# Kernel optimization log

Measured on AMD Instinct MI355X. Metric: run time of the kernel, lower is better.

The kernel has to match this reference:

```python
import jax, jax.numpy as jnp
import numpy as np

SEQ = 4096
EMBED = 1024


def setup_inputs() -> dict:
    key = jax.random.key(0)
    k1, k2 = jax.random.split(key)
    x = jax.random.normal(k1, (SEQ, EMBED), dtype=jnp.float32)
    # torch Linear(embed, 3*embed): store transposed weight so y = x @ W + b
    W = jax.random.normal(k2, (EMBED, 3 * EMBED), dtype=jnp.float32) * (1.0 / np.sqrt(EMBED))
    b = jnp.zeros((3 * EMBED,), dtype=jnp.float32)
    return {"x": x, "W": W, "b": b}


def reference(x, W, b):
    # QKV projection: [S, 3E] -> chunk along features
    qkv = x @ W + b
    q, k, v = jnp.split(qkv, 3, axis=1)  # each [S, E]
    d = q.shape[-1]
    scale = jnp.sqrt(jnp.asarray(d, dtype=x.dtype))
    logits = (q @ k.T) / scale  # [S, S]
    S = q.shape[0]
    causal = jnp.triu(jnp.ones((S, S), dtype=bool), k=1)
    logits = jnp.where(causal, -jnp.inf, logits)
    w = jax.nn.softmax(logits, axis=1)
    return w @ v  # [S, E]
```

## Files before the change

kernel.cpp:

```cpp
#include <hip/hip_runtime.h>

typedef short s16x8 __attribute__((ext_vector_type(8)));
typedef unsigned short u16;
typedef u16 u16x8 __attribute__((ext_vector_type(8)));
typedef float f32x4 __attribute__((ext_vector_type(4)));

#define SEQ 4096
#define EMBED 1024
#define NQKV 3072

static __device__ __forceinline__ u16 f2bf(float f) {
  unsigned int u = __float_as_uint(f);
  u += 0x7fffu + ((u >> 16) & 1u);
  return (u16)(u >> 16);
}
static __device__ __forceinline__ float bf2f(u16 b) {
  return __uint_as_float(((unsigned int)b) << 16);
}

static __device__ __forceinline__ f32x4 mfma16(s16x8 a, s16x8 b, f32x4 c) {
  return __builtin_amdgcn_mfma_f32_16x16x32_bf16(a, b, c, 0, 0, 0);
}

static __device__ __forceinline__ void gl2lds(const u16* g, u16* l) {
  __builtin_amdgcn_global_load_lds(
      (const __attribute__((address_space(1))) unsigned int*)g,
      (__attribute__((address_space(3))) unsigned int*)l, 16, 0, 0);
}

#define WAITVM(n) asm volatile("s_waitcnt vmcnt(" #n ")" ::: "memory")
#define LGKM0 asm volatile("s_waitcnt lgkmcnt(0)" ::: "memory")
#define BAR() asm volatile("s_waitcnt lgkmcnt(0)\n\ts_barrier" ::: "memory")

__global__ __launch_bounds__(256) void conv_x(const float* __restrict__ x,
                                              u16* __restrict__ xbf) {
  const size_t base = ((size_t)blockIdx.x * 256 + threadIdx.x) * 16;
  u16 tmp[16];
#pragma unroll
  for (int p = 0; p < 4; ++p) {
    float4 v = *reinterpret_cast<const float4*>(&x[base + p * 4]);
    tmp[p * 4 + 0] = f2bf(v.x); tmp[p * 4 + 1] = f2bf(v.y);
    tmp[p * 4 + 2] = f2bf(v.z); tmp[p * 4 + 3] = f2bf(v.w);
  }
  *reinterpret_cast<u16x8*>(&xbf[base]) = *reinterpret_cast<u16x8*>(&tmp[0]);
  *reinterpret_cast<u16x8*>(&xbf[base + 8]) = *reinterpret_cast<u16x8*>(&tmp[8]);
}

__global__ __launch_bounds__(256) void conv_wT(const float* __restrict__ W,
                                               u16* __restrict__ wT) {
  __shared__ u16 t[64][72];
  const int n0 = blockIdx.x * 64;
  const int k0 = blockIdx.y * 64;
  const int tid = threadIdx.x;
  const int rr = tid >> 3, c8 = (tid & 7) * 8;
#pragma unroll
  for (int p = 0; p < 2; ++p) {
    int r = p * 32 + rr;
    float4 a = *reinterpret_cast<const float4*>(&W[(size_t)(k0 + r) * NQKV + n0 + c8]);
    float4 b = *reinterpret_cast<const float4*>(&W[(size_t)(k0 + r) * NQKV + n0 + c8 + 4]);
    t[r][c8 + 0] = f2bf(a.x); t[r][c8 + 1] = f2bf(a.y);
    t[r][c8 + 2] = f2bf(a.z); t[r][c8 + 3] = f2bf(a.w);
    t[r][c8 + 4] = f2bf(b.x); t[r][c8 + 5] = f2bf(b.y);
    t[r][c8 + 6] = f2bf(b.z); t[r][c8 + 7] = f2bf(b.w);
  }
  __syncthreads();
#pragma unroll
  for (int p = 0; p < 2; ++p) {
    int c = p * 32 + rr;
    u16x8 v;
#pragma unroll
    for (int j = 0; j < 8; ++j) v[j] = t[c8 + j][c];
    *reinterpret_cast<u16x8*>(&wT[(size_t)(n0 + c) * EMBED + k0 + c8]) = v;
  }
}

#define GSTAGE32(dst, srcbase, stride)                                        \
  {                                                                           \
    _Pragma("unroll") for (int p_ = 0; p_ < 2; ++p_) {                        \
      gl2lds((srcbase) + (size_t)(p_ * 64 + w * 16 + (l >> 2)) * (stride) +   \
                 (l & 3) * 8,                                                 \
             (dst) + p_ * 2048 + w * 512);                                    \
    }                                                                         \
  }

#define MFMA_STEP(Acur, Bcur)                                                 \
  {                                                                           \
    s16x8 af[4], bfr[4];                                                      \
    _Pragma("unroll") for (int mb = 0; mb < 4; ++mb)                          \
        af[mb] = *reinterpret_cast<const s16x8*>(&(Acur)[(wr + mb * 16 + lr) * 32 + lg * 8]); \
    _Pragma("unroll") for (int nb = 0; nb < 4; ++nb)                          \
        bfr[nb] = *reinterpret_cast<const s16x8*>(&(Bcur)[(wc + nb * 16 + lr) * 32 + lg * 8]); \
    _Pragma("unroll") for (int mb = 0; mb < 4; ++mb)                          \
        _Pragma("unroll") for (int nb = 0; nb < 4; ++nb)                      \
            acc[mb][nb] = mfma16(af[mb], bfr[nb], acc[mb][nb]);               \
  }

__global__ __launch_bounds__(256) void qkv_gemm(const u16* __restrict__ xbf,
                                                const u16* __restrict__ wT,
                                                const float* __restrict__ bias,
                                                u16* __restrict__ qkv) {
  __shared__ u16 As[2][4096];
  __shared__ u16 Bs[2][4096];
  const int b = blockIdx.x;
  const int bs = (b & 7) * 96 + (b >> 3);
  const int bm = bs / 24, bn = bs % 24;
  const int m0 = bm * 128, n0 = bn * 128;
  const int tid = threadIdx.x;
  const int w = tid >> 6, l = tid & 63;
  const int wr = (w >> 1) * 64, wc = (w & 1) * 64;
  const int lg = l >> 4, lr = l & 15;

  f32x4 acc[4][4];
#pragma unroll
  for (int i = 0; i < 4; ++i)
#pragma unroll
    for (int j = 0; j < 4; ++j) acc[i][j] = (f32x4){0.f, 0.f, 0.f, 0.f};

  const u16* xa = xbf + (size_t)m0 * EMBED;
  const u16* wb = wT + (size_t)n0 * EMBED;

  GSTAGE32(As[0], xa, EMBED);
  GSTAGE32(Bs[0], wb, EMBED);

  for (int t = 0; t < 32; ++t) {
    const int cur = t & 1, nx = cur ^ 1;
    if (t < 31) {
      LGKM0;
      GSTAGE32(As[nx], xa + (t + 1) * 32, EMBED);
      GSTAGE32(Bs[nx], wb + (t + 1) * 32, EMBED);
      WAITVM(4);
    } else {
      WAITVM(0);
    }
    BAR();
    MFMA_STEP(As[cur], Bs[cur]);
    BAR();
  }

#pragma unroll
  for (int mb = 0; mb < 4; ++mb)
#pragma unroll
    for (int nb = 0; nb < 4; ++nb) {
      const int col = n0 + wc + nb * 16 + lr;
      const float bv = bias[col];
#pragma unroll
      for (int e = 0; e < 4; ++e) {
        const int row = m0 + wr + mb * 16 + lg * 4 + e;
        qkv[(size_t)row * NQKV + col] = f2bf(acc[mb][nb][e] + bv);
      }
    }
}

__global__ __launch_bounds__(256) void v_transpose(const u16* __restrict__ qkv,
                                                   u16* __restrict__ vT) {
  __shared__ u16 t[64][72];
  const int s0 = blockIdx.x * 64;
  const int c0 = blockIdx.y * 64;
  const int tid = threadIdx.x;
  const int rr = tid >> 3, c8 = (tid & 7) * 8;
#pragma unroll
  for (int p = 0; p < 2; ++p) {
    int r = p * 32 + rr;
    *reinterpret_cast<u16x8*>(&t[r][c8]) =
        *reinterpret_cast<const u16x8*>(&qkv[(size_t)(s0 + r) * NQKV + 2 * EMBED + c0 + c8]);
  }
  __syncthreads();
#pragma unroll
  for (int p = 0; p < 2; ++p) {
    int c = p * 32 + rr;
    u16x8 v;
#pragma unroll
    for (int j = 0; j < 8; ++j) v[j] = t[c8 + j][c];
    *reinterpret_cast<u16x8*>(&vT[(size_t)(c0 + c) * SEQ + s0 + c8]) = v;
  }
}

__global__ __launch_bounds__(256) void s_gemm(const u16* __restrict__ qkv,
                                              u16* __restrict__ Sp) {
  __shared__ u16 As[2][4096];
  __shared__ u16 Bs[2][4096];
  const int b = blockIdx.x;
  const int bs = (b & 7) * 66 + (b >> 3);
  int mt = 0, cum = 0;
  while (cum + mt + 1 <= bs) { cum += mt + 1; ++mt; }
  const int nt = bs - cum;
  const int m0 = mt * 128, n0 = nt * 128;
  const int tid = threadIdx.x;
  const int w = tid >> 6, l = tid & 63;
  const int wr = (w >> 1) * 64, wc = (w & 1) * 64;
  const int lg = l >> 4, lr = l & 15;

  f32x4 acc[4][4];
#pragma unroll
  for (int i = 0; i < 4; ++i)
#pragma unroll
    for (int j = 0; j < 4; ++j) acc[i][j] = (f32x4){0.f, 0.f, 0.f, 0.f};

  const u16* qa = qkv + (size_t)m0 * NQKV;
  const u16* kb = qkv + (size_t)n0 * NQKV + EMBED;

  GSTAGE32(As[0], qa, NQKV);
  GSTAGE32(Bs[0], kb, NQKV);

  for (int t = 0; t < 32; ++t) {
    const int cur = t & 1, nx = cur ^ 1;
    if (t < 31) {
      LGKM0;
      GSTAGE32(As[nx], qa + (t + 1) * 32, NQKV);
      GSTAGE32(Bs[nx], kb + (t + 1) * 32, NQKV);
      WAITVM(4);
    } else {
      WAITVM(0);
    }
    BAR();
    MFMA_STEP(As[cur], Bs[cur]);
    BAR();
  }

  u16* base = Sp + (size_t)bs * 16384;
#pragma unroll
  for (int mb = 0; mb < 4; ++mb)
#pragma unroll
    for (int nb = 0; nb < 4; ++nb) {
      const int cn = wc + nb * 16 + lr;
#pragma unroll
      for (int e = 0; e < 4; ++e) {
        const int rm = wr + mb * 16 + lg * 4 + e;
        base[rm * 128 + cn] = f2bf(acc[mb][nb][e] * 0.03125f);
      }
    }
}

__global__ __launch_bounds__(256) void softmax_rows(u16* __restrict__ Sp) {
  __shared__ float red[8];
  const int bid = blockIdx.x;
  const int tid = threadIdx.x;
  const int w = tid >> 6, l = tid & 63;
  const float NEG = -3.0e38f;

  for (int half = 0; half < 2; ++half) {
    const int r = half ? (4095 - bid) : bid;
    const int mt = r >> 7, rr = r & 127;
    const int Lp = (mt + 1) << 7;
    const size_t tri = (size_t)mt * (mt + 1) / 2;

    float v[16];
    float mx = NEG;
#pragma unroll
    for (int s = 0; s < 2; ++s) {
      const int j = tid * 8 + s * 2048;
      if (j < Lp) {
        const u16* p = Sp + (tri + (j >> 7)) * 16384 + rr * 128 + (j & 127);
        u16x8 xv = *reinterpret_cast<const u16x8*>(p);
#pragma unroll
        for (int e = 0; e < 8; ++e) {
          float f = (j + e <= r) ? bf2f(xv[e]) : NEG;
          v[s * 8 + e] = f;
          mx = fmaxf(mx, f);
        }
      } else {
#pragma unroll
        for (int e = 0; e < 8; ++e) v[s * 8 + e] = NEG;
      }
    }
#pragma unroll
    for (int off = 32; off >= 1; off >>= 1) mx = fmaxf(mx, __shfl_xor(mx, off, 64));
    if (l == 0) red[w] = mx;
    __syncthreads();
    mx = fmaxf(fmaxf(red[0], red[1]), fmaxf(red[2], red[3]));

    float sum = 0.f;
#pragma unroll
    for (int i = 0; i < 16; ++i) {
      float e = __expf(v[i] - mx);
      v[i] = e;
      sum += e;
    }
#pragma unroll
    for (int off = 32; off >= 1; off >>= 1) sum += __shfl_xor(sum, off, 64);
    if (l == 0) red[4 + w] = sum;
    __syncthreads();
    sum = red[4] + red[5] + red[6] + red[7];
    const float inv = 1.f / sum;

#pragma unroll
    for (int s = 0; s < 2; ++s) {
      const int j = tid * 8 + s * 2048;
      if (j < Lp) {
        u16x8 pk;
#pragma unroll
        for (int e = 0; e < 8; ++e) pk[e] = f2bf(v[s * 8 + e] * inv);
        *reinterpret_cast<u16x8*>(Sp + (tri + (j >> 7)) * 16384 + rr * 128 + (j & 127)) = pk;
      }
    }
    __syncthreads();
  }
}

__global__ __launch_bounds__(256) void pv_gemm(const u16* __restrict__ Sp,
                                               const u16* __restrict__ vT,
                                               float* __restrict__ out) {
  __shared__ u16 As[2][4096];
  __shared__ u16 Bs[2][4096];
  const int nt = blockIdx.y;
  int s81 = blockIdx.x;
  int mt = 0, cum = 0, ls = 0;
  for (;;) {
    const int ns = (mt + 8) >> 3;
    if (s81 < cum + ns) { ls = s81 - cum; break; }
    cum += ns; ++mt;
  }
  const int m0 = mt * 128, n0 = nt * 128;
  const int k0 = ls * 1024;
  const int kext = (mt + 1) * 128;
  const int kend = (k0 + 1024 < kext) ? (k0 + 1024) : kext;
  const int ksteps = (kend - k0) >> 5;
  const size_t tri = (size_t)mt * (mt + 1) / 2;

  const int tid = threadIdx.x;
  const int w = tid >> 6, l = tid & 63;
  const int wr = (w >> 1) * 64, wc = (w & 1) * 64;
  const int lg = l >> 4, lr = l & 15;

  f32x4 acc[4][4];
#pragma unroll
  for (int i = 0; i < 4; ++i)
#pragma unroll
    for (int j = 0; j < 4; ++j) acc[i][j] = (f32x4){0.f, 0.f, 0.f, 0.f};

#define PA_SRC(t) (Sp + (tri + ((k0 + (t)*32) >> 7)) * 16384 + ((k0 + (t)*32) & 127))
#define PB_SRC(t) (vT + (size_t)n0 * SEQ + k0 + (t)*32)

  GSTAGE32(As[0], PA_SRC(0), 128);
  GSTAGE32(Bs[0], PB_SRC(0), SEQ);

  for (int t = 0; t < ksteps; ++t) {
    const int cur = t & 1, nx = cur ^ 1;
    if (t + 1 < ksteps) {
      LGKM0;
      GSTAGE32(As[nx], PA_SRC(t + 1), 128);
      GSTAGE32(Bs[nx], PB_SRC(t + 1), SEQ);
      WAITVM(4);
    } else {
      WAITVM(0);
    }
    BAR();
    MFMA_STEP(As[cur], Bs[cur]);
    BAR();
  }
#undef PA_SRC
#undef PB_SRC

#pragma unroll
  for (int mb = 0; mb < 4; ++mb)
#pragma unroll
    for (int nb = 0; nb < 4; ++nb) {
      const int col = n0 + wc + nb * 16 + lr;
#pragma unroll
      for (int e = 0; e < 4; ++e) {
        const int row = m0 + wr + mb * 16 + lg * 4 + e;
        unsafeAtomicAdd(&out[(size_t)row * EMBED + col], acc[mb][nb][e]);
      }
    }
}

__global__ __launch_bounds__(512) void attn_fb(const u16* __restrict__ qkv,
                                               const u16* __restrict__ vT,
                                               float* __restrict__ out) {
  __shared__ u16 q_lds[16][1032];
  __shared__ u16 kv_lds[8][3][2048];
  __shared__ u16 p_lds[16][136];
  __shared__ float redmax[8][16];
  __shared__ float redsum[8][16];
  const int bid = blockIdx.x;
  const int tid = threadIdx.x;
  const int w = tid >> 6, l = tid & 63;
  const int lg = l >> 4, lr = l & 15;

  const int sr = l >> 4;
  const int scb = (l & 15) * 16;
  const int scolA = ((scb ^ (sr << 4)) >> 1);
  const int scolB = ((scb ^ ((4 + sr) << 4)) >> 1);
  int boff[4];
#pragma unroll
  for (int kk = 0; kk < 4; ++kk)
    boff[kk] = lr * 256 + ((kk * 64 + lg * 16) ^ ((lr & 7) << 4));

  u16* kvb[3] = {&kv_lds[w][0][0], &kv_lds[w][1][0], &kv_lds[w][2][0]};

#define STAGE_K(dc, bufp)                                                     \
  {                                                                           \
    LGKM0;                                                                    \
    const u16* g0 = qkv + (size_t)(kb + w * 16 + sr) * NQKV + EMBED + (dc) * 128; \
    gl2lds(g0 + scolA, (bufp));                                               \
    gl2lds(g0 + 4 * NQKV + scolB, (bufp) + 512);                              \
    gl2lds(g0 + 8 * NQKV + scolA, (bufp) + 1024);                             \
    gl2lds(g0 + 12 * NQKV + scolB, (bufp) + 1536);                            \
  }
#define STAGE_V(j, bufp)                                                      \
  {                                                                           \
    LGKM0;                                                                    \
    const u16* g0 = vT + (size_t)((j) * 128 + w * 16 + sr) * SEQ + kb;        \
    gl2lds(g0 + scolA, (bufp));                                               \
    gl2lds(g0 + 4 * SEQ + scolB, (bufp) + 512);                               \
    gl2lds(g0 + 8 * SEQ + scolA, (bufp) + 1024);                              \
    gl2lds(g0 + 12 * SEQ + scolB, (bufp) + 1536);                             \
  }

  const int qb = bid * 16;
  __syncthreads();
#pragma unroll
  for (int p = 0; p < 4; ++p) {
    int idx = p * 512 + tid;
    int r = idx >> 7, c = (idx & 127) * 8;
    *reinterpret_cast<u16x8*>(&q_lds[r][c]) =
        *reinterpret_cast<const u16x8*>(&qkv[(size_t)(qb + r) * NQKV + c]);
  }
  __syncthreads();
  s16x8 qf[32];
#pragma unroll
  for (int kk = 0; kk < 32; ++kk)
    qf[kk] = *reinterpret_cast<const s16x8*>(&q_lds[lr][kk * 32 + lg * 8]);

  f32x4 o_acc[8];
#pragma unroll
  for (int j = 0; j < 8; ++j) o_acc[j] = (f32x4){0.f, 0.f, 0.f, 0.f};
  float m_st[4], l_st[4];
#pragma unroll
  for (int e = 0; e < 4; ++e) { m_st[e] = -__builtin_inff(); l_st[e] = 0.f; }

  const int n_it = (qb >> 7) + 1;
  for (int it = 0; it < n_it; ++it) {
    const int kb = it << 7;
    const int kcol = kb + w * 16 + lr;

    f32x4 s = (f32x4){0.f, 0.f, 0.f, 0.f};
    STAGE_K(0, kvb[0]);
    STAGE_K(1, kvb[1]);
#pragma unroll
    for (int dc = 0; dc < 8; ++dc) {
      if (dc < 6) {
        STAGE_K(dc + 2, kvb[(dc + 2) % 3]);
      } else if (dc == 6) {
        STAGE_V(0, kvb[2]);
      } else {
        STAGE_V(1, kvb[0]);
      }
      WAITVM(8);
      u16* cur = kvb[dc % 3];
#pragma unroll
      for (int kk = 0; kk < 4; ++kk) {
        s16x8 bfr = *reinterpret_cast<const s16x8*>((const char*)cur + boff[kk]);
        s = mfma16(qf[dc * 4 + kk], bfr, s);
      }
    }

    float sv[4], mx[4];
#pragma unroll
    for (int e = 0; e < 4; ++e) {
      float v = s[e] * 0.03125f;
      sv[e] = (kcol > qb + lg * 4 + e) ? -__builtin_inff() : v;
      mx[e] = sv[e];
    }
#pragma unroll
    for (int off = 1; off < 16; off <<= 1)
#pragma unroll
      for (int e = 0; e < 4; ++e) mx[e] = fmaxf(mx[e], __shfl_xor(mx[e], off, 64));
    if (lr == 0) {
#pragma unroll
      for (int e = 0; e < 4; ++e) redmax[w][lg * 4 + e] = mx[e];
    }
    BAR();

    float m_new[4], sc[4], pv[4], rs[4];
#pragma unroll
    for (int e = 0; e < 4; ++e) {
      float m = m_st[e];
#pragma unroll
      for (int ww = 0; ww < 8; ++ww) m = fmaxf(m, redmax[ww][lg * 4 + e]);
      m_new[e] = m;
      sc[e] = __expf(m_st[e] - m);
      pv[e] = __expf(sv[e] - m);
      rs[e] = pv[e];
    }
#pragma unroll
    for (int off = 1; off < 16; off <<= 1)
#pragma unroll
      for (int e = 0; e < 4; ++e) rs[e] += __shfl_xor(rs[e], off, 64);
    if (lr == 0) {
#pragma unroll
      for (int e = 0; e < 4; ++e) redsum[w][lg * 4 + e] = rs[e];
    }
#pragma unroll
    for (int e = 0; e < 4; ++e) p_lds[lg * 4 + e][w * 16 + lr] = f2bf(pv[e]);
    BAR();

#pragma unroll
    for (int e = 0; e < 4; ++e) {
      float a2 = l_st[e] * sc[e];
#pragma unroll
      for (int ww = 0; ww < 8; ++ww) a2 += redsum[ww][lg * 4 + e];
      l_st[e] = a2;
      m_st[e] = m_new[e];
    }
#pragma unroll
    for (int j = 0; j < 8; ++j)
#pragma unroll
      for (int e = 0; e < 4; ++e) o_acc[j][e] *= sc[e];

    s16x8 pa[4];
#pragma unroll
    for (int kk = 0; kk < 4; ++kk)
      pa[kk] = *reinterpret_cast<const s16x8*>(&p_lds[lr][kk * 32 + lg * 8]);

#pragma unroll
    for (int j = 0; j < 8; ++j) {
      if (j < 6) {
        STAGE_V(j + 2, kvb[(j + 4) % 3]);
        WAITVM(8);
      } else if (j == 6) {
        WAITVM(4);
      } else {
        WAITVM(0);
      }
      u16* cur = kvb[(j + 2) % 3];
#pragma unroll
      for (int kk = 0; kk < 4; ++kk) {
        s16x8 bfr = *reinterpret_cast<const s16x8*>((const char*)cur + boff[kk]);
        o_acc[j] = mfma16(pa[kk], bfr, o_acc[j]);
      }
    }
  }

#pragma unroll
  for (int j = 0; j < 8; ++j) {
    const int col = j * 128 + w * 16 + lr;
#pragma unroll
    for (int e = 0; e < 4; ++e)
      out[(size_t)(qb + lg * 4 + e) * EMBED + col] = o_acc[j][e] / l_st[e];
  }
#undef STAGE_K
#undef STAGE_V
}

extern "C" void kernel_launch(void* const* d_in, const int* in_sizes, int n_in,
                              void* d_out, int out_size, void* d_ws, size_t ws_size,
                              hipStream_t stream) {
  (void)in_sizes; (void)n_in; (void)out_size;
  const float* x = (const float*)d_in[0];
  const float* W = (const float*)d_in[1];
  const float* bias = (const float*)d_in[2];
  float* out = (float*)d_out;

  u16* qkv = (u16*)d_ws;
  u16* vT = qkv + (size_t)SEQ * NQKV;
  u16* xbf = vT;
  u16* wT = (u16*)d_out;
  u16* Sp = (u16*)((char*)d_ws + (32u << 20));

  const size_t need = (32u << 20) + (size_t)528 * 16384 * 2;

  conv_x<<<(SEQ * EMBED) / (256 * 16), 256, 0, stream>>>(x, xbf);
  conv_wT<<<dim3(NQKV / 64, EMBED / 64), 256, 0, stream>>>(W, wT);
  qkv_gemm<<<(SEQ / 128) * (NQKV / 128), 256, 0, stream>>>(xbf, wT, bias, qkv);
  v_transpose<<<dim3(SEQ / 64, EMBED / 64), 256, 0, stream>>>(qkv, vT);

  if (ws_size >= need) {
    s_gemm<<<528, 256, 0, stream>>>(qkv, Sp);
    softmax_rows<<<2048, 256, 0, stream>>>(Sp);
    hipMemsetAsync(d_out, 0, (size_t)SEQ * EMBED * sizeof(float), stream);
    pv_gemm<<<dim3(80, 8), 256, 0, stream>>>(Sp, vT, out);
  } else {
    attn_fb<<<SEQ / 16, 512, 0, stream>>>(qkv, vT, out);
  }
}
```

Measured before the change: 158.0 us.

## Triple-buffer GEMM K-loops and split PV reduction into finer K chunks

```diff
diff --git a/kernel.cpp b/kernel.cpp
--- a/kernel.cpp
+++ b/kernel.cpp
@@ -95,12 +95,35 @@
             acc[mb][nb] = mfma16(af[mb], bfr[nb], acc[mb][nb]);               \
   }
 
+#define KLOOP(n, SRC_A, SA_STRIDE, SRC_B, SB_STRIDE)                          \
+  GSTAGE32(As[0], SRC_A(0), SA_STRIDE);                                       \
+  GSTAGE32(Bs[0], SRC_B(0), SB_STRIDE);                                       \
+  GSTAGE32(As[1], SRC_A(1), SA_STRIDE);                                       \
+  GSTAGE32(Bs[1], SRC_B(1), SB_STRIDE);                                       \
+  for (int t = 0; t < (n); ++t) {                                             \
+    const int cur = t % 3;                                                    \
+    if (t + 2 < (n)) {                                                        \
+      LGKM0;                                                                  \
+      const int nx = (t + 2) % 3;                                             \
+      GSTAGE32(As[nx], SRC_A(t + 2), SA_STRIDE);                              \
+      GSTAGE32(Bs[nx], SRC_B(t + 2), SB_STRIDE);                              \
+      WAITVM(8);                                                              \
+    } else if (t + 1 < (n)) {                                                 \
+      WAITVM(4);                                                              \
+    } else {                                                                  \
+      WAITVM(0);                                                              \
+    }                                                                         \
+    BAR();                                                                    \
+    MFMA_STEP(As[cur], Bs[cur]);                                              \
+    BAR();                                                                    \
+  }
+
 __global__ __launch_bounds__(256) void qkv_gemm(const u16* __restrict__ xbf,
                                                 const u16* __restrict__ wT,
                                                 const float* __restrict__ bias,
                                                 u16* __restrict__ qkv) {
-  __shared__ u16 As[2][4096];
-  __shared__ u16 Bs[2][4096];
+  __shared__ u16 As[3][4096];
+  __shared__ u16 Bs[3][4096];
   const int b = blockIdx.x;
   const int bs = (b & 7) * 96 + (b >> 3);
   const int bm = bs / 24, bn = bs % 24;
@@ -118,24 +141,11 @@
 
   const u16* xa = xbf + (size_t)m0 * EMBED;
   const u16* wb = wT + (size_t)n0 * EMBED;
-
-  GSTAGE32(As[0], xa, EMBED);
-  GSTAGE32(Bs[0], wb, EMBED);
-
-  for (int t = 0; t < 32; ++t) {
-    const int cur = t & 1, nx = cur ^ 1;
-    if (t < 31) {
-      LGKM0;
-      GSTAGE32(As[nx], xa + (t + 1) * 32, EMBED);
-      GSTAGE32(Bs[nx], wb + (t + 1) * 32, EMBED);
-      WAITVM(4);
-    } else {
-      WAITVM(0);
-    }
-    BAR();
-    MFMA_STEP(As[cur], Bs[cur]);
-    BAR();
-  }
+#define QA_SRC(t) (xa + (t) * 32)
+#define QB_SRC(t) (wb + (t) * 32)
+  KLOOP(32, QA_SRC, EMBED, QB_SRC, EMBED);
+#undef QA_SRC
+#undef QB_SRC
 
 #pragma unroll
   for (int mb = 0; mb < 4; ++mb)
@@ -177,8 +187,8 @@
 
 __global__ __launch_bounds__(256) void s_gemm(const u16* __restrict__ qkv,
                                               u16* __restrict__ Sp) {
-  __shared__ u16 As[2][4096];
-  __shared__ u16 Bs[2][4096];
+  __shared__ u16 As[3][4096];
+  __shared__ u16 Bs[3][4096];
   const int b = blockIdx.x;
   const int bs = (b & 7) * 66 + (b >> 3);
   int mt = 0, cum = 0;
@@ -198,24 +208,11 @@
 
   const u16* qa = qkv + (size_t)m0 * NQKV;
   const u16* kb = qkv + (size_t)n0 * NQKV + EMBED;
-
-  GSTAGE32(As[0], qa, NQKV);
-  GSTAGE32(Bs[0], kb, NQKV);
-
-  for (int t = 0; t < 32; ++t) {
-    const int cur = t & 1, nx = cur ^ 1;
-    if (t < 31) {
-      LGKM0;
-      GSTAGE32(As[nx], qa + (t + 1) * 32, NQKV);
-      GSTAGE32(Bs[nx], kb + (t + 1) * 32, NQKV);
-      WAITVM(4);
-    } else {
-      WAITVM(0);
-    }
-    BAR();
-    MFMA_STEP(As[cur], Bs[cur]);
-    BAR();
-  }
+#define SA_SRC(t) (qa + (t) * 32)
+#define SB_SRC(t) (kb + (t) * 32)
+  KLOOP(32, SA_SRC, NQKV, SB_SRC, NQKV);
+#undef SA_SRC
+#undef SB_SRC
 
   u16* base = Sp + (size_t)bs * 16384;
 #pragma unroll
@@ -300,20 +297,20 @@
 __global__ __launch_bounds__(256) void pv_gemm(const u16* __restrict__ Sp,
                                                const u16* __restrict__ vT,
                                                float* __restrict__ out) {
-  __shared__ u16 As[2][4096];
-  __shared__ u16 Bs[2][4096];
+  __shared__ u16 As[3][4096];
+  __shared__ u16 Bs[3][4096];
   const int nt = blockIdx.y;
-  int s81 = blockIdx.x;
+  int sx = blockIdx.x;
   int mt = 0, cum = 0, ls = 0;
   for (;;) {
-    const int ns = (mt + 8) >> 3;
-    if (s81 < cum + ns) { ls = s81 - cum; break; }
+    const int ns = (mt + 4) >> 2;
+    if (sx < cum + ns) { ls = sx - cum; break; }
     cum += ns; ++mt;
   }
   const int m0 = mt * 128, n0 = nt * 128;
-  const int k0 = ls * 1024;
+  const int k0 = ls * 512;
   const int kext = (mt + 1) * 128;
-  const int kend = (k0 + 1024 < kext) ? (k0 + 1024) : kext;
+  const int kend = (k0 + 512 < kext) ? (k0 + 512) : kext;
   const int ksteps = (kend - k0) >> 5;
   const size_t tri = (size_t)mt * (mt + 1) / 2;
 
@@ -330,24 +327,7 @@
 
 #define PA_SRC(t) (Sp + (tri + ((k0 + (t)*32) >> 7)) * 16384 + ((k0 + (t)*32) & 127))
 #define PB_SRC(t) (vT + (size_t)n0 * SEQ + k0 + (t)*32)
-
-  GSTAGE32(As[0], PA_SRC(0), 128);
-  GSTAGE32(Bs[0], PB_SRC(0), SEQ);
-
-  for (int t = 0; t < ksteps; ++t) {
-    const int cur = t & 1, nx = cur ^ 1;
-    if (t + 1 < ksteps) {
-      LGKM0;
-      GSTAGE32(As[nx], PA_SRC(t + 1), 128);
-      GSTAGE32(Bs[nx], PB_SRC(t + 1), SEQ);
-      WAITVM(4);
-    } else {
-      WAITVM(0);
-    }
-    BAR();
-    MFMA_STEP(As[cur], Bs[cur]);
-    BAR();
-  }
+  KLOOP(ksteps, PA_SRC, 128, PB_SRC, SEQ);
 #undef PA_SRC
 #undef PB_SRC
 
@@ -569,7 +549,7 @@
     s_gemm<<<528, 256, 0, stream>>>(qkv, Sp);
     softmax_rows<<<2048, 256, 0, stream>>>(Sp);
     hipMemsetAsync(d_out, 0, (size_t)SEQ * EMBED * sizeof(float), stream);
-    pv_gemm<<<dim3(80, 8), 256, 0, stream>>>(Sp, vT, out);
+    pv_gemm<<<dim3(144, 8), 256, 0, stream>>>(Sp, vT, out);
   } else {
     attn_fb<<<SEQ / 16, 512, 0, stream>>>(qkv, vT, out);
   }
```

Measured after the change: 180.4 us. 14.2% more time.
